# Optimization experiments

Measured on AMD Instinct MI355X. Metric: run time of the kernel, lower is better.

Reference implementation:

```python
import math
import jax, jax.numpy as jnp
import numpy as np

B, S, D = 8, 1024, 768
N_HEAD, D_HEAD = 12, 64


def setup_inputs() -> dict:
    key = jax.random.key(0)
    k1, k2, k3, k4, k5 = jax.random.split(key, 5)
    return {
        "x": jax.random.normal(k1, (B, S, D), dtype=jnp.float32),
        "W_qkv": jax.random.normal(k2, (D, 3 * D), dtype=jnp.float32) * 0.02,
        "b_qkv": jax.random.normal(k3, (3 * D,), dtype=jnp.float32) * 0.02,
        "W_proj": jax.random.normal(k4, (D, D), dtype=jnp.float32) * 0.02,
        "b_proj": jax.random.normal(k5, (D,), dtype=jnp.float32) * 0.02,
    }


def reference(x, W_qkv, b_qkv, W_proj, b_proj):
    b, s, d = x.shape
    qkv = x @ W_qkv + b_qkv                      # [B,S,3D]
    q, k, v = jnp.split(qkv, 3, axis=-1)
    # [B,S,D] -> [B,H,S,Dh]
    q = q.reshape(b, s, N_HEAD, D_HEAD).transpose(0, 2, 1, 3)
    k = k.reshape(b, s, N_HEAD, D_HEAD).transpose(0, 2, 1, 3)
    v = v.reshape(b, s, N_HEAD, D_HEAD).transpose(0, 2, 1, 3)
    scores = jnp.einsum("bhqd,bhkd->bhqk", q, k) / math.sqrt(D_HEAD)
    causal = jnp.tril(jnp.ones((s, s), dtype=bool))  # [S,S]
    scores = jnp.where(causal[None, None], scores, -jnp.inf)
    probs = jax.nn.softmax(scores, axis=-1)
    out = jnp.einsum("bhqk,bhkd->bhqd", probs, v)    # [B,H,S,Dh]
    out = out.transpose(0, 2, 1, 3).reshape(b, s, d)
    out = out @ W_proj + b_proj
    return out, (k, v)
```

## Files before the change

### kernel.cpp

```cpp
#include <hip/hip_runtime.h>

typedef unsigned short u16;
typedef unsigned int   u32;
typedef short bf16x8 __attribute__((ext_vector_type(8)));
typedef float f32x4  __attribute__((ext_vector_type(4)));
typedef float f32x16 __attribute__((ext_vector_type(16)));
typedef u16   u16x4  __attribute__((ext_vector_type(4)));
typedef u16   u16x8  __attribute__((ext_vector_type(8)));
typedef u32   u32x2  __attribute__((ext_vector_type(2)));
typedef u32   u32x4  __attribute__((ext_vector_type(4)));

#define DEV __device__ __forceinline__
#define MFMA32(A,B,C) __builtin_amdgcn_mfma_f32_32x32x16_bf16(A,B,C,0,0,0)

DEV u16 f2bf(float f) {
  u32 u = __builtin_bit_cast(u32, f);
  u32 r = (u + 0x7FFFu + ((u >> 16) & 1u)) >> 16;
  return (u16)r;
}
DEV u32 pack2(float lo, float hi) {
  return (u32)f2bf(lo) | ((u32)f2bf(hi) << 16);
}
DEV void gll16(const u16* g, u16* l) {
  __builtin_amdgcn_global_load_lds((const __attribute__((address_space(1))) u32*)g,
                                   (__attribute__((address_space(3))) u32*)l,
                                   16, 0, 0);
}

__global__ __launch_bounds__(256)
void cvt_bf16(const float* __restrict__ in, u16* __restrict__ out, int n8) {
  int i = blockIdx.x * 256 + threadIdx.x;
  if (i >= n8) return;
  float4 a = ((const float4*)in)[2*i];
  float4 b = ((const float4*)in)[2*i+1];
  u16x8 o;
  o[0]=f2bf(a.x); o[1]=f2bf(a.y); o[2]=f2bf(a.z); o[3]=f2bf(a.w);
  o[4]=f2bf(b.x); o[5]=f2bf(b.y); o[6]=f2bf(b.z); o[7]=f2bf(b.w);
  *(u16x8*)(out + (size_t)i*8) = o;
}

__global__ __launch_bounds__(256)
void transpose_w(const float* __restrict__ in, u16* __restrict__ out, int R, int C) {
  __shared__ float t64[64][65];
  const int r0 = blockIdx.x*64, c0 = blockIdx.y*64;
  const int tr = threadIdx.x >> 4, tc = (threadIdx.x & 15) * 4;
  #pragma unroll
  for (int i = 0; i < 4; ++i) {
    int r = i*16 + tr;
    float4 v = *(const float4*)(in + (size_t)(r0 + r)*C + c0 + tc);
    t64[r][tc+0]=v.x; t64[r][tc+1]=v.y; t64[r][tc+2]=v.z; t64[r][tc+3]=v.w;
  }
  __syncthreads();
  #pragma unroll
  for (int i = 0; i < 4; ++i) {
    int r = i*16 + tr;
    u16x4 ov;
    ov[0]=f2bf(t64[tc+0][r]); ov[1]=f2bf(t64[tc+1][r]);
    ov[2]=f2bf(t64[tc+2][r]); ov[3]=f2bf(t64[tc+3][r]);
    *(u16x4*)(out + (size_t)(c0 + r)*R + r0 + tc) = ov;
  }
}

template<int MODE>
__global__ __launch_bounds__(256)
void gemm_k(const u16* __restrict__ A, const u16* __restrict__ Bt,
            const float* __restrict__ bias,
            float* __restrict__ o0, float* __restrict__ o1,
            u16* __restrict__ qo, u16* __restrict__ ko)
{
  constexpr int K = 768;
  constexpr int NT = 24;
  __shared__ u16 As[3 * 128 * 32];
  __shared__ u16 Bs[3 * 128 * 32];
  const int tid = threadIdx.x;
  const int w  = tid >> 6, ln = tid & 63;
  const int wr = w >> 1,  wc = w & 1;
  const int g  = ln >> 4, c  = ln & 15;
  const int tm = blockIdx.x * 128, tn = blockIdx.y * 128;

  const f32x4 fzero = {0.f, 0.f, 0.f, 0.f};
  f32x4 acc[4][4];
  #pragma unroll
  for (int i = 0; i < 4; ++i)
    #pragma unroll
    for (int j = 0; j < 4; ++j) acc[i][j] = fzero;

  const int srow = w*32 + (ln >> 2);
  const int seg  = (ln & 3) * 8;
  const u16* ga = A  + (size_t)(tm + srow)*K + seg;
  const u16* gb = Bt + (size_t)(tn + srow)*K + seg;
  const int woff = __builtin_amdgcn_readfirstlane(w * 1024);

#define STAGE(P, K0) do {                              \
    u16* la_ = As + (P)*4096 + woff;                   \
    u16* lb_ = Bs + (P)*4096 + woff;                   \
    gll16(ga + (K0),          la_);                    \
    gll16(ga + (K0) + 16*K,   la_ + 512);              \
    gll16(gb + (K0),          lb_);                    \
    gll16(gb + (K0) + 16*K,   lb_ + 512);              \
  } while (0)

  STAGE(0, 0);
  STAGE(1, 32);
  int p = 0;
  for (int t = 0; t < NT; ++t) {
    if (t + 2 < NT) {
      int pn = p + 2; if (pn >= 3) pn -= 3;
      STAGE(pn, (t + 2) * 32);
      asm volatile("s_waitcnt vmcnt(8)" ::: "memory");
    } else if (t + 1 < NT) {
      asm volatile("s_waitcnt vmcnt(4)" ::: "memory");
    } else {
      asm volatile("s_waitcnt vmcnt(0)" ::: "memory");
    }
    __builtin_amdgcn_s_barrier();

    const u16* Ab = As + p*4096;
    const u16* Bb = Bs + p*4096;
    bf16x8 af[4], bfv[4];
    #pragma unroll
    for (int mi = 0; mi < 4; ++mi)
      af[mi] = *(const bf16x8*)&Ab[(wr*64 + mi*16 + c)*32 + g*8];
    #pragma unroll
    for (int ni = 0; ni < 4; ++ni)
      bfv[ni] = *(const bf16x8*)&Bb[(wc*64 + ni*16 + c)*32 + g*8];
    #pragma unroll
    for (int mi = 0; mi < 4; ++mi)
      #pragma unroll
      for (int ni = 0; ni < 4; ++ni)
        acc[mi][ni] = __builtin_amdgcn_mfma_f32_16x16x32_bf16(af[mi], bfv[ni], acc[mi][ni], 0, 0, 0);

    asm volatile("" ::: "memory");
    __builtin_amdgcn_s_barrier();
    ++p; if (p == 3) p = 0;
  }
#undef STAGE

  const int tnw = tn + wc*64;
  float bias_v[4];
  #pragma unroll
  for (int ni = 0; ni < 4; ++ni) bias_v[ni] = bias[tnw + ni*16 + c];

  if (MODE == 1) {
    #pragma unroll
    for (int mi = 0; mi < 4; ++mi)
      #pragma unroll
      for (int r = 0; r < 4; ++r) {
        int mrow = tm + wr*64 + mi*16 + 4*g + r;
        float* op = o0 + (size_t)mrow*768 + tnw + c;
        #pragma unroll
        for (int ni = 0; ni < 4; ++ni)
          op[ni*16] = acc[mi][ni][r] + bias_v[ni];
      }
  } else {
    const float QSCALE = 0.18033688f;
    const int part = tnw / 768;
    const int hh   = (tnw - part*768) >> 6;
    #pragma unroll
    for (int mi = 0; mi < 4; ++mi)
      #pragma unroll
      for (int r = 0; r < 4; ++r) {
        int mrow = tm + wr*64 + mi*16 + 4*g + r;
        int bI = mrow >> 10, s = mrow & 1023;
        size_t base = (((size_t)(bI*12 + hh) << 10) + (size_t)s) * 64 + c;
        #pragma unroll
        for (int ni = 0; ni < 4; ++ni) {
          float v = acc[mi][ni][r] + bias_v[ni];
          size_t idx = base + ni*16;
          if (part == 0)      { qo[idx] = f2bf(v * QSCALE); }
          else if (part == 1) { o0[idx] = v; ko[idx] = f2bf(v); }
          else                { o1[idx] = v; }
        }
      }
  }
}

__global__ __launch_bounds__(256)
void transpose_v(const float* __restrict__ vin, u16* __restrict__ vt) {
  __shared__ float t64[64][65];
  const int bh = blockIdx.x, s0 = blockIdx.y * 64;
  const int tr = threadIdx.x >> 4, tc = (threadIdx.x & 15) * 4;
  const float* src = vin + ((size_t)bh*1024 + s0) * 64;
  #pragma unroll
  for (int i = 0; i < 4; ++i) {
    int r = i*16 + tr;
    float4 v = *(const float4*)(src + (size_t)r*64 + tc);
    t64[r][tc+0]=v.x; t64[r][tc+1]=v.y; t64[r][tc+2]=v.z; t64[r][tc+3]=v.w;
  }
  __syncthreads();
  u16* dst = vt + (size_t)bh*64*1024 + s0;
  #pragma unroll
  for (int i = 0; i < 4; ++i) {
    int d = i*16 + tr;
    u16x4 ov;
    ov[0]=f2bf(t64[tc+0][d]); ov[1]=f2bf(t64[tc+1][d]);
    ov[2]=f2bf(t64[tc+2][d]); ov[3]=f2bf(t64[tc+3][d]);
    *(u16x4*)(dst + (size_t)d*1024 + tc) = ov;
  }
}

#define LOADT(KF, VF, TI) do {                                              \
  const int k32_ = (TI) << 5;                                               \
  const u16* kp_ = kb + hbase + (size_t)(k32_ + cl) * 64 + (hf << 3);       \
  KF[0] = *(const bf16x8*)(kp_);       KF[1] = *(const bf16x8*)(kp_ + 16);  \
  KF[2] = *(const bf16x8*)(kp_ + 32);  KF[3] = *(const bf16x8*)(kp_ + 48);  \
  const u16* vp_ = vt + hbase + (size_t)cl * 1024 + k32_ + (hf << 3);       \
  VF[0] = *(const bf16x8*)(vp_);           VF[1] = *(const bf16x8*)(vp_ + 16); \
  VF[2] = *(const bf16x8*)(vp_ + 32768);   VF[3] = *(const bf16x8*)(vp_ + 32768 + 16); \
} while (0)

#define TILE(KF, VF, DIAG) do {                                             \
  f32x16 st_ = 0.f;                                                         \
  st_ = MFMA32(KF[0], qf[0], st_); st_ = MFMA32(KF[1], qf[1], st_);         \
  st_ = MFMA32(KF[2], qf[2], st_); st_ = MFMA32(KF[3], qf[3], st_);         \
  float x_[16];                                                             \
  _Pragma("unroll")                                                         \
  for (int r = 0; r < 16; ++r) x_[r] = st_[r];                              \
  if (DIAG) {                                                               \
    _Pragma("unroll")                                                       \
    for (int r = 0; r < 16; ++r)                                            \
      if (((r & 3) + 8 * (r >> 2) + (hf << 2)) > cl) x_[r] = -1e30f;        \
  }                                                                         \
  float y_[8];                                                              \
  _Pragma("unroll")                                                         \
  for (int r = 0; r < 8; ++r) y_[r] = fmaxf(x_[r], x_[r + 8]);              \
  _Pragma("unroll")                                                         \
  for (int r = 0; r < 4; ++r) y_[r] = fmaxf(y_[r], y_[r + 4]);              \
  float mt_ = fmaxf(fmaxf(y_[0], y_[1]), fmaxf(y_[2], y_[3]));              \
  mt_ = fmaxf(mt_, __shfl_xor(mt_, 32));                                    \
  if (!__all(mt_ - m <= 8.0f)) {                         \
    float mn_ = fmaxf(m, mt_);                                              \
    float sc_ = exp2f(m - mn_);                                             \
    _Pragma("unroll")                                                       \
    for (int r = 0; r < 16; ++r) { o0[r] *= sc_; o1[r] *= sc_; }            \
    lsum *= sc_; m = mn_;                                                   \
  }                                                                         \
  float p_[16]; float rs_ = 0.f;                                            \
  _Pragma("unroll")                                                         \
  for (int r = 0; r < 16; ++r) { p_[r] = exp2f(x_[r] - m); rs_ += p_[r]; }  \
  rs_ += __shfl_xor(rs_, 32);                                               \
  lsum += rs_;                                                              \
  u32 ww_[8], xw_[8];                                                       \
  _Pragma("unroll")                                                         \
  for (int i = 0; i < 8; ++i) ww_[i] = pack2(p_[2*i], p_[2*i+1]);           \
  _Pragma("unroll")                                                         \
  for (int i = 0; i < 8; ++i) xw_[i] = (u32)__shfl_xor((int)ww_[i], 32);    \
  u32x4 b0_, b1_;                                                           \
  b0_[0] = hf ? xw_[2] : ww_[0]; b0_[1] = hf ? xw_[3] : ww_[1];             \
  b0_[2] = hf ? ww_[2] : xw_[0]; b0_[3] = hf ? ww_[3] : xw_[1];             \
  b1_[0] = hf ? xw_[6] : ww_[4]; b1_[1] = hf ? xw_[7] : ww_[5];             \
  b1_[2] = hf ? ww_[6] : xw_[4]; b1_[3] = hf ? ww_[7] : xw_[5];             \
  bf16x8 pb0_ = __builtin_bit_cast(bf16x8, b0_);                            \
  bf16x8 pb1_ = __builtin_bit_cast(bf16x8, b1_);                            \
  o0 = MFMA32(VF[0], pb0_, o0); o0 = MFMA32(VF[1], pb1_, o0);               \
  o1 = MFMA32(VF[2], pb0_, o1); o1 = MFMA32(VF[3], pb1_, o1);               \
} while (0)

__global__ __launch_bounds__(256)
void attn_k(const u16* __restrict__ qb, const u16* __restrict__ kb,
            const u16* __restrict__ vt, u16* __restrict__ attnb)
{
  const int w = threadIdx.x >> 6, ln = threadIdx.x & 63;
  const int u = blockIdx.x * 4 + w;
  const int head = u % 96;
  const int qt = 31 - (u / 96);
  const int q0 = qt << 5;
  const int b = head / 12, h = head % 12;
  const int cl = ln & 31, hf = ln >> 5;
  const size_t hbase = (size_t)head << 16;

  const u16* Qp = qb + hbase + (size_t)(q0 + cl) * 64 + (hf << 3);
  bf16x8 qf[4];
  qf[0] = *(const bf16x8*)(Qp);       qf[1] = *(const bf16x8*)(Qp + 16);
  qf[2] = *(const bf16x8*)(Qp + 32);  qf[3] = *(const bf16x8*)(Qp + 48);

  f32x16 o0 = 0.f, o1 = 0.f;
  float m = -1e30f, lsum = 0.f;

  bf16x8 kA[4], vA[4], kB[4], vB[4];
  const int nfull = qt;
  LOADT(kA, vA, 0);
  int t = 0;
  while (t < nfull) {
    LOADT(kB, vB, t + 1);
    TILE(kA, vA, 0);
    ++t;
    if (t >= nfull) break;
    LOADT(kA, vA, t + 1);
    TILE(kB, vB, 0);
    ++t;
  }
  if (nfull & 1) TILE(kB, vB, 1);
  else           TILE(kA, vA, 1);

  const float rinv = 1.0f / lsum;
  const size_t obase = ((size_t)(b * 1024 + q0 + cl)) * 768 + h * 64;
  #pragma unroll
  for (int grp = 0; grp < 4; ++grp) {
    u32x2 s0, s1;
    s0[0] = pack2(o0[grp*4+0]*rinv, o0[grp*4+1]*rinv);
    s0[1] = pack2(o0[grp*4+2]*rinv, o0[grp*4+3]*rinv);
    *(u32x2*)(attnb + obase + grp*8 + (hf << 2)) = s0;
    s1[0] = pack2(o1[grp*4+0]*rinv, o1[grp*4+1]*rinv);
    s1[1] = pack2(o1[grp*4+2]*rinv, o1[grp*4+3]*rinv);
    *(u32x2*)(attnb + obase + 32 + grp*8 + (hf << 2)) = s1;
  }
}

extern "C" void kernel_launch(void* const* d_in, const int* in_sizes, int n_in,
                              void* d_out, int out_size, void* d_ws, size_t ws_size,
                              hipStream_t stream)
{
  (void)in_sizes; (void)n_in; (void)out_size; (void)ws_size;
  const float* x     = (const float*)d_in[0];
  const float* Wqkv  = (const float*)d_in[1];
  const float* bqkv  = (const float*)d_in[2];
  const float* Wproj = (const float*)d_in[3];
  const float* bproj = (const float*)d_in[4];
  float* out  = (float*)d_out;
  float* outK = out + 6291456;
  float* outV = out + 2*6291456;

  char* ws = (char*)d_ws;
  u16* xb    = (u16*)ws; ws += 12582912;
  u16* wqt   = (u16*)ws; ws += 3538944;
  u16* wpt   = (u16*)ws; ws += 1179648;
  u16* qbuf  = (u16*)ws; ws += 12582912;
  u16* kbuf  = (u16*)ws; ws += 12582912;
  u16* vtb   = (u16*)ws; ws += 12582912;
  u16* attnb = (u16*)ws; ws += 12582912;

  cvt_bf16   <<<3072, 256, 0, stream>>>(x, xb, 786432);
  transpose_w<<<dim3(12, 36), 256, 0, stream>>>(Wqkv,  wqt, 768, 2304);
  transpose_w<<<dim3(12, 12), 256, 0, stream>>>(Wproj, wpt, 768, 768);
  gemm_k<0>  <<<dim3(64, 18), 256, 0, stream>>>(xb, wqt, bqkv, outK, outV, qbuf, kbuf);
  transpose_v<<<dim3(96, 16), 256, 0, stream>>>(outV, vtb);
  attn_k     <<<768, 256, 0, stream>>>(qbuf, kbuf, vtb, attnb);
  gemm_k<1>  <<<dim3(64, 6),  256, 0, stream>>>(attnb, wpt, bproj, out, nullptr, nullptr, nullptr);
}
```

Baseline: 154.4 us.

## Fuse V transpose into QKV GEMM epilogue and switch to double-buffered LDS pipeline

The QKV GEMM epilogue now writes V directly as transposed bf16 (packing four consecutive sequence rows per store), so the separate transpose_v kernel and its extra read of the fp32 V output go away. The GEMM main loop also moves from a three-stage to a two-stage LDS buffer with a full vmcnt(0) wait and one barrier per iteration, and adds sched_barriers. This cuts LDS use but exposes more global-load latency per K step.

Result: no change. 152.3 us (-1.3%).

```diff
diff --git a/kernel.cpp b/kernel.cpp
--- a/kernel.cpp
+++ b/kernel.cpp
@@ -66,12 +66,12 @@
 void gemm_k(const u16* __restrict__ A, const u16* __restrict__ Bt,
             const float* __restrict__ bias,
             float* __restrict__ o0, float* __restrict__ o1,
-            u16* __restrict__ qo, u16* __restrict__ ko)
+            u16* __restrict__ qo, u16* __restrict__ ko, u16* __restrict__ vto)
 {
   constexpr int K = 768;
   constexpr int NT = 24;
-  __shared__ u16 As[3 * 128 * 32];
-  __shared__ u16 Bs[3 * 128 * 32];
+  __shared__ u16 As[2 * 4096];
+  __shared__ u16 Bs[2 * 4096];
   const int tid = threadIdx.x;
   const int w  = tid >> 6, ln = tid & 63;
   const int wr = w >> 1,  wc = w & 1;
@@ -101,22 +101,15 @@
   } while (0)
 
   STAGE(0, 0);
-  STAGE(1, 32);
-  int p = 0;
+  asm volatile("s_waitcnt vmcnt(0)" ::: "memory");
+  __builtin_amdgcn_s_barrier();
+  __builtin_amdgcn_sched_barrier(0);
+
+  int cur = 0;
   for (int t = 0; t < NT; ++t) {
-    if (t + 2 < NT) {
-      int pn = p + 2; if (pn >= 3) pn -= 3;
-      STAGE(pn, (t + 2) * 32);
-      asm volatile("s_waitcnt vmcnt(8)" ::: "memory");
-    } else if (t + 1 < NT) {
-      asm volatile("s_waitcnt vmcnt(4)" ::: "memory");
-    } else {
-      asm volatile("s_waitcnt vmcnt(0)" ::: "memory");
-    }
-    __builtin_amdgcn_s_barrier();
-
-    const u16* Ab = As + p*4096;
-    const u16* Bb = Bs + p*4096;
+    if (t + 1 < NT) STAGE(cur ^ 1, (t + 1) * 32);
+    const u16* Ab = As + cur*4096;
+    const u16* Bb = Bs + cur*4096;
     bf16x8 af[4], bfv[4];
     #pragma unroll
     for (int mi = 0; mi < 4; ++mi)
@@ -129,10 +122,11 @@
       #pragma unroll
       for (int ni = 0; ni < 4; ++ni)
         acc[mi][ni] = __builtin_amdgcn_mfma_f32_16x16x32_bf16(af[mi], bfv[ni], acc[mi][ni], 0, 0, 0);
-
-    asm volatile("" ::: "memory");
+    __builtin_amdgcn_sched_barrier(0);
+    if (t + 1 < NT) asm volatile("s_waitcnt vmcnt(0)" ::: "memory");
     __builtin_amdgcn_s_barrier();
-    ++p; if (p == 3) p = 0;
+    __builtin_amdgcn_sched_barrier(0);
+    cur ^= 1;
   }
 #undef STAGE
 
@@ -155,47 +149,39 @@
   } else {
     const float QSCALE = 0.18033688f;
     const int part = tnw / 768;
-    const int hh   = (tnw - part*768) >> 6;
-    #pragma unroll
-    for (int mi = 0; mi < 4; ++mi)
+    const int hh   = ((tnw - part*768) >> 6);
+    #pragma unroll
+    for (int mi = 0; mi < 4; ++mi) {
+      const int mbase = tm + wr*64 + mi*16 + 4*g;
+      const int bI = mbase >> 10, s = mbase & 1023;
+      const size_t hb = (size_t)(bI*12 + hh) << 10;
+      float v[4][4];
+      #pragma unroll
+      for (int r = 0; r < 4; ++r)
+        #pragma unroll
+        for (int ni = 0; ni < 4; ++ni)
+          v[r][ni] = acc[mi][ni][r] + bias_v[ni];
       #pragma unroll
       for (int r = 0; r < 4; ++r) {
-        int mrow = tm + wr*64 + mi*16 + 4*g + r;
-        int bI = mrow >> 10, s = mrow & 1023;
-        size_t base = (((size_t)(bI*12 + hh) << 10) + (size_t)s) * 64 + c;
+        size_t base = (hb + s + r) * 64 + c;
         #pragma unroll
         for (int ni = 0; ni < 4; ++ni) {
-          float v = acc[mi][ni][r] + bias_v[ni];
           size_t idx = base + ni*16;
-          if (part == 0)      { qo[idx] = f2bf(v * QSCALE); }
-          else if (part == 1) { o0[idx] = v; ko[idx] = f2bf(v); }
-          else                { o1[idx] = v; }
+          if (part == 0)      { qo[idx] = f2bf(v[r][ni] * QSCALE); }
+          else if (part == 1) { o0[idx] = v[r][ni]; ko[idx] = f2bf(v[r][ni]); }
+          else                { o1[idx] = v[r][ni]; }
         }
       }
-  }
-}
-
-__global__ __launch_bounds__(256)
-void transpose_v(const float* __restrict__ vin, u16* __restrict__ vt) {
-  __shared__ float t64[64][65];
-  const int bh = blockIdx.x, s0 = blockIdx.y * 64;
-  const int tr = threadIdx.x >> 4, tc = (threadIdx.x & 15) * 4;
-  const float* src = vin + ((size_t)bh*1024 + s0) * 64;
-  #pragma unroll
-  for (int i = 0; i < 4; ++i) {
-    int r = i*16 + tr;
-    float4 v = *(const float4*)(src + (size_t)r*64 + tc);
-    t64[r][tc+0]=v.x; t64[r][tc+1]=v.y; t64[r][tc+2]=v.z; t64[r][tc+3]=v.w;
-  }
-  __syncthreads();
-  u16* dst = vt + (size_t)bh*64*1024 + s0;
-  #pragma unroll
-  for (int i = 0; i < 4; ++i) {
-    int d = i*16 + tr;
-    u16x4 ov;
-    ov[0]=f2bf(t64[tc+0][d]); ov[1]=f2bf(t64[tc+1][d]);
-    ov[2]=f2bf(t64[tc+2][d]); ov[3]=f2bf(t64[tc+3][d]);
-    *(u16x4*)(dst + (size_t)d*1024 + tc) = ov;
+      if (part == 2) {
+        #pragma unroll
+        for (int ni = 0; ni < 4; ++ni) {
+          u32x2 pk;
+          pk[0] = pack2(v[0][ni], v[1][ni]);
+          pk[1] = pack2(v[2][ni], v[3][ni]);
+          *(u32x2*)(vto + (hb << 6) + (size_t)(ni*16 + c)*1024 + s) = pk;
+        }
+      }
+    }
   }
 }
 
@@ -333,8 +319,7 @@
   cvt_bf16   <<<3072, 256, 0, stream>>>(x, xb, 786432);
   transpose_w<<<dim3(12, 36), 256, 0, stream>>>(Wqkv,  wqt, 768, 2304);
   transpose_w<<<dim3(12, 12), 256, 0, stream>>>(Wproj, wpt, 768, 768);
-  gemm_k<0>  <<<dim3(64, 18), 256, 0, stream>>>(xb, wqt, bqkv, outK, outV, qbuf, kbuf);
-  transpose_v<<<dim3(96, 16), 256, 0, stream>>>(outV, vtb);
+  gemm_k<0>  <<<dim3(64, 18), 256, 0, stream>>>(xb, wqt, bqkv, outK, outV, qbuf, kbuf, vtb);
   attn_k     <<<768, 256, 0, stream>>>(qbuf, kbuf, vtb, attnb);
-  gemm_k<1>  <<<dim3(64, 6),  256, 0, stream>>>(attnb, wpt, bproj, out, nullptr, nullptr, nullptr);
-}
+  gemm_k<1>  <<<dim3(64, 6),  256, 0, stream>>>(attnb, wpt, bproj, out, nullptr, nullptr, nullptr, nullptr);
+}
```
